# Kernel tuning notes

Measured on AMD Instinct MI355X. Metric: run time of the kernel, lower is better.

Reference implementation:

```python
import jax, jax.numpy as jnp
import numpy as np

N = 200000   # num_nodes
D = 64       # embedding_dims
B = 4096     # batch of target nodes (batched per-edge processing)
K = 128      # padded in-neighbor count per target
W = 20       # window_size (history deque length)
H = 128      # hidden_size


def setup_inputs() -> dict:
    key = jax.random.key(0)
    ks = jax.random.split(key, 14)
    return {
        "adj_time": jax.random.uniform(ks[0], (N,), jnp.float32),          # last-seen times in [0,1)
        "gc": jax.random.uniform(ks[1], (N,), jnp.float32),                 # per-node centrality scalar (dict_gc)
        "cur_time": jnp.ones((1,), jnp.float32),                            # current event time (>= all stored times)
        "neigh_mask": jnp.ones((B, K), jnp.float32),                        # 1 = valid neighbor slot
        "hist_feat": jax.random.normal(ks[2], (B, W, 2 * D), jnp.float32),  # feature_dict[...]['feature'] deque
        "hist_time": jax.random.uniform(ks[3], (B, W), jnp.float32),        # feature_dict[...]['time'] deque
        "t2v_w": jax.random.normal(ks[4], (D,), jnp.float32),               # Time2Vec('cos') weights
        "t2v_b": jax.random.normal(ks[5], (D,), jnp.float32),
        "node_w": jax.random.normal(ks[6], (D,), jnp.float32),              # linear_node: Linear(1, D)
        "node_b": jax.random.normal(ks[7], (D,), jnp.float32),
        "att_w": jax.random.normal(ks[8], (2 * D,), jnp.float32),           # Attention: score = cat(a,b) @ w + b
        "att_b": jax.random.normal(ks[9], (1,), jnp.float32),
        "weight": jax.random.normal(ks[10], (H, 4 * D), jnp.float32) * 0.05,
        "targets": jax.random.randint(ks[11], (B,), 0, N),
        "neigh_idx": jax.random.randint(ks[12], (B, K), 0, N),
    }


def reference(adj_time, gc, cur_time, neigh_mask, hist_feat, hist_time,
              t2v_w, t2v_b, node_w, node_b, att_w, att_b, weight,
              targets, neigh_idx):
    t = cur_time[0]

    def node_encoding(idx):
        # Time2Vec('cos'): first channel linear, rest cos(w*dt+b)
        dt = jnp.abs(t - adj_time[idx])[..., None]            # [..., 1]
        phase = t2v_w * dt + t2v_b                            # [..., D]
        tv = jnp.concatenate([phase[..., :1], jnp.cos(phase[..., 1:])], axis=-1)
        feat = jax.nn.relu(tv + gc[idx][..., None] * node_w + node_b)
        # F.normalize (L2 over feature dim)
        return feat / jnp.maximum(jnp.linalg.norm(feat, axis=-1, keepdims=True), 1e-12)

    tgt_feat = node_encoding(targets)       # [B, D]
    ngh_feat = node_encoding(neigh_idx)     # [B, K, D]

    # Decayer(2, 'log'): time_score = 1 / (2 * log(e + dt))
    time_score = 1.0 / (2.0 * jnp.log(jnp.e + (t - adj_time[neigh_idx])))   # [B, K]
    # Attention score between target and each neighbor encoding
    att = (tgt_feat @ att_w[:D])[:, None] \
        + jnp.einsum("bkd,d->bk", ngh_feat, att_w[D:]) + att_b[0]           # [B, K]
    score = jax.nn.leaky_relu(time_score + att, 0.01) * neigh_mask          # [B, K]
    neigh_agg = jnp.einsum("bk,bkd->bd", score, ngh_feat)                   # [B, D]

    combined = jnp.concatenate([tgt_feat, neigh_agg], axis=-1)              # [B, 2D]

    # History aggregation with Decayer(2, 'rev'): w = 1 / (2 * (1 + dt))
    hist_w = 1.0 / (2.0 * (1.0 + (t - hist_time)))                          # [B, W]
    hist_agg = jnp.einsum("bw,bwd->bd", hist_w, hist_feat)                  # [B, 2D]

    feat4 = jnp.concatenate([hist_agg, combined], axis=-1)                  # [B, 4D]
    return jax.nn.relu(feat4 @ weight.T)                                    # [B, H]
```

## Files before the change

### kernel.cpp

```cpp
#include <hip/hip_runtime.h>
#include <math.h>

#define NN 200000
#define DD 64
#define BB 4096
#define KK 128
#define WW 20
#define HH 128
#define TPB 512
#define RPB 4

#define INV2PI 0.15915494309189535f

__device__ __forceinline__ float fast_rcp(float x) { return __builtin_amdgcn_rcpf(x); }
__device__ __forceinline__ float fast_rsq(float x) { return __builtin_amdgcn_rsqf(x); }

__global__ __launch_bounds__(512, 8) void fused(
    const float* __restrict__ adj_time, const float* __restrict__ gc,
    const float* __restrict__ cur_time, const float* __restrict__ neigh_mask,
    const float* __restrict__ hist_feat, const float* __restrict__ hist_time,
    const float* __restrict__ t2v_w, const float* __restrict__ t2v_b,
    const float* __restrict__ node_w, const float* __restrict__ node_b,
    const float* __restrict__ att_w, const float* __restrict__ att_b,
    const float* __restrict__ weight,
    const int* __restrict__ targets, const int* __restrict__ neigh_idx,
    float* __restrict__ out)
{
    const int b0   = blockIdx.x * RPB;
    const int tid  = threadIdx.x;
    const int lane = tid & 63;
    const int wv   = tid >> 6;

    __shared__ float4 dtg[RPB * KK];
    __shared__ float  stL[RPB];
    __shared__ float  p3p[RPB][DD];
    __shared__ float  tile[RPB * 256];

    const float t = cur_time[0];

    const int   slot = tid;
    const int   idx  = neigh_idx[b0 * KK + slot];
    const float m    = neigh_mask[b0 * KK + slot];
    const float at   = adj_time[idx];
    const float g    = gc[idx];
    const float dt   = fabsf(t - at);
    const float ts   = fast_rcp(2.0f * __logf(2.71828182845904523536f + (t - at)));
    dtg[slot] = make_float4(dt, g, 0.f, 0.f);

    if (tid >= 384) {
        const int r  = (tid >> 5) & 3;
        const int c4 = tid & 31;
        const float*  ht = hist_time + (size_t)(b0 + r) * WW;
        const float4* hf = (const float4*)(hist_feat + (size_t)(b0 + r) * WW * 128) + c4;
        float4 s4 = make_float4(0.f, 0.f, 0.f, 0.f);
#pragma unroll 4
        for (int w = 0; w < WW; ++w) {
            float  hw = fast_rcp(2.0f * (1.0f + (t - ht[w])));
            float4 v  = hf[w * 32];
            s4.x = fmaf(hw, v.x, s4.x);
            s4.y = fmaf(hw, v.y, s4.y);
            s4.z = fmaf(hw, v.z, s4.z);
            s4.w = fmaf(hw, v.w, s4.w);
        }
        *(float4*)(tile + r * 256 + c4 * 4) = s4;
    }

    if (wv < RPB) {
        int   tg  = targets[b0 + wv];
        float dtT = fabsf(t - adj_time[tg]);
        float gT  = gc[tg];
        float ph  = fmaf(t2v_w[lane], dtT, t2v_b[lane]);
        float cv  = __builtin_amdgcn_cosf(ph * INV2PI);
        float tv_ = (lane == 0) ? ph : cv;
        float f   = fmaxf(tv_ + fmaf(gT, node_w[lane], node_b[lane]), 0.f);
        float ss  = f * f;
#pragma unroll
        for (int off = 32; off; off >>= 1) ss += __shfl_xor(ss, off, 64);
        float invn = fast_rsq(fmaxf(ss, 1e-24f));
        float tfn  = f * invn;
        float sdt  = tfn * att_w[lane];
#pragma unroll
        for (int off = 32; off; off >>= 1) sdt += __shfl_xor(sdt, off, 64);
        if (lane == 0) stL[wv] = sdt;
        tile[wv * 256 + 128 + lane] = tfn;
    }

    float s2, sd;
    {
        {
            float ph = fmaf(t2v_w[0], dt, t2v_b[0]);
            float f  = fmaxf(ph + fmaf(g, node_w[0], node_b[0]), 0.f);
            s2 = f * f;
            sd = f * att_w[64];
        }
#pragma unroll 4
        for (int d = 1; d < 64; ++d) {
            float ph = fmaf(t2v_w[d], dt, t2v_b[d]);
            float cv = __builtin_amdgcn_cosf(ph * INV2PI);
            float f  = fmaxf(cv + fmaf(g, node_w[d], node_b[d]), 0.f);
            s2 = fmaf(f, f, s2);
            sd = fmaf(f, att_w[64 + d], sd);
        }
    }
    __syncthreads();

    {
        float invn = fast_rsq(fmaxf(s2, 1e-24f));
        float sc   = ts + stL[slot >> 7] + sd * invn + att_b[0];
        sc = (sc > 0.f) ? sc : 0.01f * sc;
        dtg[slot].z = sc * m * invn;
    }
    __syncthreads();

    const int r3   = wv >> 1;
    const int half = wv & 1;
    float acc3 = 0.f;
    {
        float scn = (lane == 0) ? 1.f : INV2PI;
        float pw  = t2v_w[lane] * scn;
        float pb  = t2v_b[lane] * scn;
        float nw  = node_w[lane];
        float nb2 = node_b[lane];
        const int base = r3 * KK + half * 64;
#pragma unroll 4
        for (int k = 0; k < 64; ++k) {
            float4 dgw = dtg[base + k];
            float  ph  = fmaf(pw, dgw.x, pb);
            float  cv  = __builtin_amdgcn_cosf(ph);
            float  tv_ = lane ? cv : ph;
            float  f   = fmaxf(tv_ + fmaf(dgw.y, nw, nb2), 0.f);
            acc3 = fmaf(dgw.z, f, acc3);
        }
    }
    if (half) p3p[r3][lane] = acc3;
    __syncthreads();
    if (!half) tile[r3 * 256 + 192 + lane] = acc3 + p3p[r3][lane];
    __syncthreads();

    const int h  = tid & 127;
    const int sq = tid >> 7;
    const float4* w4 = (const float4*)weight + h * 64 + sq * 16;
    const int jb = sq * 64;
    float a0 = 0.f, a1 = 0.f, a2 = 0.f, a3 = 0.f;
#pragma unroll 4
    for (int j4 = 0; j4 < 16; ++j4) {
        float4 w  = w4[j4];
        const int jo = jb + j4 * 4;
        float4 f0 = *(const float4*)(tile + 0 * 256 + jo);
        float4 f1 = *(const float4*)(tile + 1 * 256 + jo);
        float4 f2 = *(const float4*)(tile + 2 * 256 + jo);
        float4 f3 = *(const float4*)(tile + 3 * 256 + jo);
        a0 += w.x * f0.x + w.y * f0.y + w.z * f0.z + w.w * f0.w;
        a1 += w.x * f1.x + w.y * f1.y + w.z * f1.z + w.w * f1.w;
        a2 += w.x * f2.x + w.y * f2.y + w.z * f2.z + w.w * f2.w;
        a3 += w.x * f3.x + w.y * f3.y + w.z * f3.z + w.w * f3.w;
    }

    float* prow = (float*)dtg;
    prow[(0 * 4 + sq) * 128 + h] = a0;
    prow[(1 * 4 + sq) * 128 + h] = a1;
    prow[(2 * 4 + sq) * 128 + h] = a2;
    prow[(3 * 4 + sq) * 128 + h] = a3;
    __syncthreads();
    {
        const int r2 = tid >> 7;
        float s = prow[(r2 * 4 + 0) * 128 + h] + prow[(r2 * 4 + 1) * 128 + h]
                + prow[(r2 * 4 + 2) * 128 + h] + prow[(r2 * 4 + 3) * 128 + h];
        out[(size_t)(b0 + r2) * 128 + h] = fmaxf(s, 0.f);
    }
}

extern "C" void kernel_launch(void* const* d_in, const int* in_sizes, int n_in,
                              void* d_out, int out_size, void* d_ws, size_t ws_size,
                              hipStream_t stream) {
    const float* adj_time  = (const float*)d_in[0];
    const float* gc        = (const float*)d_in[1];
    const float* cur_time  = (const float*)d_in[2];
    const float* neigh_mask= (const float*)d_in[3];
    const float* hist_feat = (const float*)d_in[4];
    const float* hist_time = (const float*)d_in[5];
    const float* t2v_w     = (const float*)d_in[6];
    const float* t2v_b     = (const float*)d_in[7];
    const float* node_w    = (const float*)d_in[8];
    const float* node_b    = (const float*)d_in[9];
    const float* att_w     = (const float*)d_in[10];
    const float* att_b     = (const float*)d_in[11];
    const float* weight    = (const float*)d_in[12];
    const int*   targets   = (const int*)d_in[13];
    const int*   neigh_idx = (const int*)d_in[14];

    float* out = (float*)d_out;

    fused<<<BB / RPB, TPB, 0, stream>>>(adj_time, gc, cur_time, neigh_mask,
                                        hist_feat, hist_time, t2v_w, t2v_b,
                                        node_w, node_b, att_w, att_b, weight,
                                        targets, neigh_idx, out);
}
```

Baseline: 138.4 us.

## Compute neighbor encodings once with 8-lane splits and DPP reductions

Previously each neighbor's 64-dimensional Time2Vec encoding was evaluated twice: once per slot thread to get the norm and attention score, and again per dimension lane for the weighted aggregation. Now each neighbor is handled by 8 lanes that each compute 8 dimensions. They keep the values in registers, reduce the norm and score with DPP and shuffle ops, then accumulate the weighted features directly. This roughly halves the cosine and FMA work and removes one block barrier. In exchange it adds cross-lane reductions, per-wave partial buffers in LDS, and higher register pressure, so the occupancy hint in launch_bounds drops from 8 to 4.

```diff
diff --git a/kernel.cpp b/kernel.cpp
--- a/kernel.cpp
+++ b/kernel.cpp
@@ -15,7 +15,17 @@
 __device__ __forceinline__ float fast_rcp(float x) { return __builtin_amdgcn_rcpf(x); }
 __device__ __forceinline__ float fast_rsq(float x) { return __builtin_amdgcn_rsqf(x); }
 
-__global__ __launch_bounds__(512, 8) void fused(
+template <int CTRL>
+__device__ __forceinline__ float dpp_add(float x) {
+    int y = __builtin_amdgcn_update_dpp(0, __float_as_int(x), CTRL, 0xF, 0xF, true);
+    return x + __int_as_float(y);
+}
+#define DPP_XOR1  0xB1
+#define DPP_XOR2  0x4E
+#define DPP_HMIRR 0x141
+#define DPP_ROR8  0x128
+
+__global__ __launch_bounds__(512, 4) void fused(
     const float* __restrict__ adj_time, const float* __restrict__ gc,
     const float* __restrict__ cur_time, const float* __restrict__ neigh_mask,
     const float* __restrict__ hist_feat, const float* __restrict__ hist_time,
@@ -33,19 +43,41 @@
 
     __shared__ float4 dtg[RPB * KK];
     __shared__ float  stL[RPB];
-    __shared__ float  p3p[RPB][DD];
+    __shared__ float  part[RPB][8][DD];
     __shared__ float  tile[RPB * 256];
 
     const float t = cur_time[0];
 
-    const int   slot = tid;
-    const int   idx  = neigh_idx[b0 * KK + slot];
-    const float m    = neigh_mask[b0 * KK + slot];
-    const float at   = adj_time[idx];
-    const float g    = gc[idx];
-    const float dt   = fabsf(t - at);
-    const float ts   = fast_rcp(2.0f * __logf(2.71828182845904523536f + (t - at)));
-    dtg[slot] = make_float4(dt, g, 0.f, 0.f);
+    const int dg = lane >> 3;
+    const int d0 = dg * 8;
+    float pw[8], pb[8], nw[8], nb[8], aw[8];
+    {
+        float4 a0 = *(const float4*)(t2v_w + d0),  a1 = *(const float4*)(t2v_w + d0 + 4);
+        float4 b0_ = *(const float4*)(t2v_b + d0), b1 = *(const float4*)(t2v_b + d0 + 4);
+        float4 c0 = *(const float4*)(node_w + d0), c1 = *(const float4*)(node_w + d0 + 4);
+        float4 e0 = *(const float4*)(node_b + d0), e1 = *(const float4*)(node_b + d0 + 4);
+        float4 w0 = *(const float4*)(att_w + 64 + d0), w1 = *(const float4*)(att_w + 64 + d0 + 4);
+        pw[0]=a0.x*INV2PI; pw[1]=a0.y*INV2PI; pw[2]=a0.z*INV2PI; pw[3]=a0.w*INV2PI;
+        pw[4]=a1.x*INV2PI; pw[5]=a1.y*INV2PI; pw[6]=a1.z*INV2PI; pw[7]=a1.w*INV2PI;
+        pb[0]=b0_.x*INV2PI; pb[1]=b0_.y*INV2PI; pb[2]=b0_.z*INV2PI; pb[3]=b0_.w*INV2PI;
+        pb[4]=b1.x*INV2PI; pb[5]=b1.y*INV2PI; pb[6]=b1.z*INV2PI; pb[7]=b1.w*INV2PI;
+        nw[0]=c0.x; nw[1]=c0.y; nw[2]=c0.z; nw[3]=c0.w; nw[4]=c1.x; nw[5]=c1.y; nw[6]=c1.z; nw[7]=c1.w;
+        nb[0]=e0.x; nb[1]=e0.y; nb[2]=e0.z; nb[3]=e0.w; nb[4]=e1.x; nb[5]=e1.y; nb[6]=e1.z; nb[7]=e1.w;
+        aw[0]=w0.x; aw[1]=w0.y; aw[2]=w0.z; aw[3]=w0.w; aw[4]=w1.x; aw[5]=w1.y; aw[6]=w1.z; aw[7]=w1.w;
+    }
+    const float ow0 = t2v_w[0], ob0 = t2v_b[0];
+    const float ab  = att_b[0];
+    const bool  isd0 = (dg == 0);
+
+    {
+        const int   idx = neigh_idx[b0 * KK + tid];
+        const float m   = neigh_mask[b0 * KK + tid];
+        const float at  = adj_time[idx];
+        const float g   = gc[idx];
+        const float dt  = fabsf(t - at);
+        const float ts  = fast_rcp(2.0f * __logf(2.71828182845904523536f + (t - at)));
+        dtg[tid] = make_float4(dt, g, ts, m);
+    }
 
     if (tid >= 384) {
         const int r  = (tid >> 5) & 3;
@@ -84,57 +116,67 @@
         if (lane == 0) stL[wv] = sdt;
         tile[wv * 256 + 128 + lane] = tfn;
     }
-
-    float s2, sd;
-    {
-        {
-            float ph = fmaf(t2v_w[0], dt, t2v_b[0]);
-            float f  = fmaxf(ph + fmaf(g, node_w[0], node_b[0]), 0.f);
-            s2 = f * f;
-            sd = f * att_w[64];
-        }
-#pragma unroll 4
-        for (int d = 1; d < 64; ++d) {
-            float ph = fmaf(t2v_w[d], dt, t2v_b[d]);
-            float cv = __builtin_amdgcn_cosf(ph * INV2PI);
-            float f  = fmaxf(cv + fmaf(g, node_w[d], node_b[d]), 0.f);
-            s2 = fmaf(f, f, s2);
-            sd = fmaf(f, att_w[64 + d], sd);
-        }
-    }
-    __syncthreads();
-
-    {
-        float invn = fast_rsq(fmaxf(s2, 1e-24f));
-        float sc   = ts + stL[slot >> 7] + sd * invn + att_b[0];
-        sc = (sc > 0.f) ? sc : 0.01f * sc;
-        dtg[slot].z = sc * m * invn;
-    }
-    __syncthreads();
-
-    const int r3   = wv >> 1;
-    const int half = wv & 1;
-    float acc3 = 0.f;
-    {
-        float scn = (lane == 0) ? 1.f : INV2PI;
-        float pw  = t2v_w[lane] * scn;
-        float pb  = t2v_b[lane] * scn;
-        float nw  = node_w[lane];
-        float nb2 = node_b[lane];
-        const int base = r3 * KK + half * 64;
-#pragma unroll 4
-        for (int k = 0; k < 64; ++k) {
-            float4 dgw = dtg[base + k];
-            float  ph  = fmaf(pw, dgw.x, pb);
-            float  cv  = __builtin_amdgcn_cosf(ph);
-            float  tv_ = lane ? cv : ph;
-            float  f   = fmaxf(tv_ + fmaf(dgw.y, nw, nb2), 0.f);
-            acc3 = fmaf(dgw.z, f, acc3);
-        }
-    }
-    if (half) p3p[r3][lane] = acc3;
-    __syncthreads();
-    if (!half) tile[r3 * 256 + 192 + lane] = acc3 + p3p[r3][lane];
+    __syncthreads();
+
+#pragma unroll
+    for (int r = 0; r < RPB; ++r) {
+        const float stv = stL[r];
+        float acc[8] = {0.f, 0.f, 0.f, 0.f, 0.f, 0.f, 0.f, 0.f};
+#pragma unroll
+        for (int pass = 0; pass < 2; ++pass) {
+            const float4 dgw = dtg[r * KK + pass * 64 + wv * 8 + (lane & 7)];
+            const float dts = dgw.x, gs = dgw.y, tss = dgw.z, ms = dgw.w;
+            float f[8], s2, sd;
+            {
+                float ph  = fmaf(pw[0], dts, pb[0]);
+                float cv  = __builtin_amdgcn_cosf(ph);
+                float lin = fmaf(ow0, dts, ob0);
+                float tv_ = isd0 ? lin : cv;
+                float fv  = fmaxf(tv_ + fmaf(gs, nw[0], nb[0]), 0.f);
+                f[0] = fv; s2 = fv * fv; sd = fv * aw[0];
+            }
+#pragma unroll
+            for (int i = 1; i < 8; ++i) {
+                float ph = fmaf(pw[i], dts, pb[i]);
+                float cv = __builtin_amdgcn_cosf(ph);
+                float fv = fmaxf(cv + fmaf(gs, nw[i], nb[i]), 0.f);
+                f[i] = fv;
+                s2 = fmaf(fv, fv, s2);
+                sd = fmaf(fv, aw[i], sd);
+            }
+            s2 = dpp_add<DPP_ROR8>(s2);
+            s2 += __shfl_xor(s2, 16, 64);
+            s2 += __shfl_xor(s2, 32, 64);
+            sd = dpp_add<DPP_ROR8>(sd);
+            sd += __shfl_xor(sd, 16, 64);
+            sd += __shfl_xor(sd, 32, 64);
+            float invn = fast_rsq(fmaxf(s2, 1e-24f));
+            float sc   = tss + stv + sd * invn + ab;
+            sc = (sc > 0.f) ? sc : 0.01f * sc;
+            float wk = sc * ms * invn;
+#pragma unroll
+            for (int i = 0; i < 8; ++i) acc[i] = fmaf(wk, f[i], acc[i]);
+        }
+#pragma unroll
+        for (int i = 0; i < 8; ++i) {
+            acc[i] = dpp_add<DPP_XOR1>(acc[i]);
+            acc[i] = dpp_add<DPP_XOR2>(acc[i]);
+            acc[i] = dpp_add<DPP_HMIRR>(acc[i]);
+        }
+        if ((lane & 7) == 0) {
+#pragma unroll
+            for (int i = 0; i < 8; ++i) part[r][wv][d0 + i] = acc[i];
+        }
+    }
+    __syncthreads();
+
+    if (tid < 256) {
+        const int r = tid >> 6, d = tid & 63;
+        float s = 0.f;
+#pragma unroll
+        for (int w = 0; w < 8; ++w) s += part[r][w][d];
+        tile[r * 256 + 192 + d] = s;
+    }
     __syncthreads();
 
     const int h  = tid & 127;
```

After: 136.5 us. No clear change (-1.4%).
